# Kernel optimization log

Measured on AMD Instinct MI355X. Metric: run time of the kernel, lower is better.

Reference implementation:

```python
import jax, jax.numpy as jnp
import numpy as np

NUM_HEADS = 16
HEAD_DIM = 64
PATCH_NUMS = [1, 2, 3, 4, 5, 6, 8, 10, 13, 16, 32]
MAX_SCALE_MUL = float(np.log(100.0))


def precompute_freqs_cis(dim, patch_nums, theta=10000.0):
    # Returns [L, dim//2, 2] (cos, sin) pairs; matches torch.polar construction.
    freqs = 1.0 / theta ** (np.arange(0, dim, 4)[: dim // 4].astype(np.float32) / dim)  # [dim//4]
    tx, ty = [], []
    grid = 32.0
    for p in patch_nums:
        ix, iy = np.meshgrid(np.arange(p), np.arange(p), indexing="ij")  # torch default 'ij'
        tx.append(ix.flatten().astype(np.float32) / p * grid)
        ty.append(iy.flatten().astype(np.float32) / p * grid)
    tx = np.concatenate(tx)
    ty = np.concatenate(ty)
    ang = np.concatenate([np.outer(tx, freqs), np.outer(ty, freqs)], axis=1).astype(np.float32)  # [L, dim//2]
    return np.stack([np.cos(ang), np.sin(ang)], axis=-1)  # [L, dim//2, 2]


FREQS_CIS_CROSS = jnp.asarray(precompute_freqs_cis(HEAD_DIM, [12]))  # [144, 32, 2]


def _rope(x, cis):
    # x: [B, H, S, D]; cis: [S, D//2, 2] -> complex multiply on (even, odd) pairs.
    B, H, S, D = x.shape
    xr = x.reshape(B, H, S, D // 2, 2)
    a, b = xr[..., 0], xr[..., 1]
    c = cis[..., 0][None, None]  # [1,1,S,D//2]
    d = cis[..., 1][None, None]
    return jnp.stack([a * c - b * d, a * d + b * c], axis=-1).reshape(B, H, S, D)


def setup_inputs() -> dict:
    key = jax.random.key(0)
    ks = jax.random.split(key, 6)
    B, C, Ck, Lk = 8, 1024, 1024, 144
    fc = precompute_freqs_cis(HEAD_DIM, PATCH_NUMS)
    L = fc.shape[0]  # 1704
    return {
        "x": jax.random.normal(ks[0], (B, L, C), jnp.float32),
        "y": jax.random.normal(ks[1], (B, Lk, Ck), jnp.float32),
        "freqs_cis": jnp.asarray(fc),
        "attn_bias": jax.random.normal(ks[2], (1, 1, L, Lk), jnp.float32) * 0.1,
        "Wq": jax.random.normal(ks[3], (C, C), jnp.float32) * 0.02,
        "q_bias": jnp.zeros((C,), jnp.float32),
        "Wkv": jax.random.normal(ks[4], (2 * C, Ck), jnp.float32) * 0.02,
        "v_bias": jnp.zeros((C,), jnp.float32),
        "Wproj": jax.random.normal(ks[5], (C, C), jnp.float32) * 0.02,
        "b_proj": jnp.zeros((C,), jnp.float32),
        "scale_mul": jnp.full((1, NUM_HEADS, 1, 1), np.log(4.0), jnp.float32),
    }


def reference(x, y, freqs_cis, attn_bias, Wq, q_bias, Wkv, v_bias, Wproj, b_proj, scale_mul):
    B, L, C = x.shape
    H, D = NUM_HEADS, HEAD_DIM
    Lk = y.shape[1]
    # fused QKV projections (k bias is the zero buffer)
    q = (x @ Wq.T + q_bias).reshape(B, L, H, D).transpose(0, 2, 1, 3)  # [B,H,L,D]
    kv_bias = jnp.concatenate([jnp.zeros_like(v_bias), v_bias])
    kv = (y @ Wkv.T + kv_bias).reshape(B, Lk, 2, H, D)
    k = kv[:, :, 0].transpose(0, 2, 1, 3)  # [B,H,Lk,D]
    v = kv[:, :, 1].transpose(0, 2, 1, 3)
    # attn_l2_norm path: scale = 1, per-head learned multiplier
    sm = jnp.exp(jnp.minimum(scale_mul, MAX_SCALE_MUL))  # [1,H,1,1]
    q = q / jnp.maximum(jnp.linalg.norm(q, axis=-1, keepdims=True), 1e-12) * sm
    k = k / jnp.maximum(jnp.linalg.norm(k, axis=-1, keepdims=True), 1e-12)
    # inline RoPE (cross freqs recomputed from 12x12 grid every forward in the original)
    q = _rope(q, freqs_cis)
    k = _rope(k, FREQS_CIS_CROSS)
    # manual (non-flash) masked attention, scale = 1 due to l2 norm
    logits = jnp.einsum("bhld,bhkd->bhlk", q, k) + attn_bias
    attn = jax.nn.softmax(logits, axis=-1)
    oup = jnp.einsum("bhlk,bhkd->bhld", attn, v).transpose(0, 2, 1, 3).reshape(B, L, C)
    return oup @ Wproj.T + b_proj
```

## Files before the change

### kernel.cpp

```cpp
#include <hip/hip_runtime.h>

using u16 = unsigned short;
using u32 = unsigned int;

typedef __bf16 bf16x8 __attribute__((ext_vector_type(8)));
typedef float  f32x4  __attribute__((ext_vector_type(4)));
typedef _Float16 f16;
typedef _Float16 f16x4 __attribute__((ext_vector_type(4)));
typedef _Float16 f16x8 __attribute__((ext_vector_type(8)));
typedef u16 u16x4 __attribute__((ext_vector_type(4)));

__device__ __forceinline__ float b2f(u16 u) { return __uint_as_float(((u32)u) << 16); }
__device__ __forceinline__ u16 f2b(float f) {
    u32 u = __float_as_uint(f);
    return (u16)((u + 0x7FFFu + ((u >> 16) & 1u)) >> 16);
}

__device__ __forceinline__ void async_cp16(void* lds, const void* g) {
    __builtin_amdgcn_global_load_lds(
        (const __attribute__((address_space(1))) u32*)g,
        (__attribute__((address_space(3))) u32*)lds, 16, 0, 0);
}

__device__ __forceinline__ void split4_store(const float* src, u16* hi, u16* lo, int i) {
    f32x4 v = reinterpret_cast<const f32x4*>(src)[i];
    u16x4 H, L;
#pragma unroll
    for (int j = 0; j < 4; j++) {
        u16 hb = f2b(v[j]);
        H[j] = hb;
        L[j] = f2b(v[j] - b2f(hb));
    }
    reinterpret_cast<u16x4*>(hi)[i] = H;
    reinterpret_cast<u16x4*>(lo)[i] = L;
}

__global__ __launch_bounds__(256) void prep(const float* __restrict__ x,
                                            const float* __restrict__ Wq,
                                            const float* __restrict__ Wp,
                                            const float* __restrict__ y,
                                            const float* __restrict__ Wkv,
                                            f16* __restrict__ xf,
                                            f16* __restrict__ wqhi, f16* __restrict__ wqlo,
                                            f16* __restrict__ wph,
                                            u16* __restrict__ yhi, u16* __restrict__ ylo,
                                            u16* __restrict__ wkhi, u16* __restrict__ wklo,
                                            int nx4, int nw4, int ny4, int nwk4) {
    int i = blockIdx.x * 256 + threadIdx.x;
    if (i < nx4) {
        f32x4 v = reinterpret_cast<const f32x4*>(x)[i];
        f16x4 h = {(f16)v[0], (f16)v[1], (f16)v[2], (f16)v[3]};
        reinterpret_cast<f16x4*>(xf)[i] = h;
    } else if (i < nx4 + nw4) {
        int k = i - nx4;
        f32x4 v = reinterpret_cast<const f32x4*>(Wq)[k];
        f16x4 H, L;
#pragma unroll
        for (int j = 0; j < 4; j++) {
            f16 hb = (f16)v[j];
            H[j] = hb;
            L[j] = (f16)(v[j] - (float)hb);
        }
        reinterpret_cast<f16x4*>(wqhi)[k] = H;
        reinterpret_cast<f16x4*>(wqlo)[k] = L;
    } else if (i < nx4 + 2 * nw4) {
        int k = i - nx4 - nw4;
        f32x4 v = reinterpret_cast<const f32x4*>(Wp)[k];
        f16x4 h = {(f16)v[0], (f16)v[1], (f16)v[2], (f16)v[3]};
        reinterpret_cast<f16x4*>(wph)[k] = h;
    } else if (i < nx4 + 2 * nw4 + ny4) {
        int k = i - nx4 - 2 * nw4;
        split4_store(y, yhi, ylo, k);
    } else {
        int k = i - nx4 - 2 * nw4 - ny4;
        if (k < nwk4) split4_store(Wkv, wkhi, wklo, k);
    }
}

__device__ __forceinline__ void remap852(int j, int& mt, int& sg) {
    if (j < 832) {
        int a = j >> 5, rem = j & 31;
        mt = a * 8 + (rem & 7);
        sg = rem >> 3;
    } else {
        int rem = j - 832;
        mt = 208 + rem % 5;
        sg = rem / 5;
    }
}

__global__ __launch_bounds__(256) void gemm_q(const f16* __restrict__ xf,
                                              const f16* __restrict__ whi,
                                              const f16* __restrict__ wlo,
                                              const float* __restrict__ qb,
                                              const float* __restrict__ fc,
                                              const float* __restrict__ smul,
                                              f16* __restrict__ qout) {
    const int K = 1024, L = 1704;
    __shared__ f16 xs[2][2][64][64];
    int tid = threadIdx.x;
    int lane = tid & 63, wv = tid >> 6;
    int mt, hg;
    remap852(blockIdx.x, mt, hg);
    int h  = hg * 4 + wv;
    int lr = lane & 15, quad = lane >> 4;
    long m0 = (long)mt * 64;

    int r0 = tid >> 3, c0 = tid & 7;
    int s1i = tid + 256;
    int r1 = s1i >> 3, c1 = s1i & 7;
    const f16* srcx0 = xf + (m0 + r0) * K + ((c0 ^ (r0 & 7)) * 8);
    const f16* srcx1 = xf + (m0 + r1) * K + ((c1 ^ (r1 & 7)) * 8);
    f16* dx[2][2][2];
#pragma unroll
    for (int b = 0; b < 2; b++)
#pragma unroll
        for (int hh = 0; hh < 2; hh++) {
            dx[b][hh][0] = &xs[b][hh][r0][c0 * 8];
            dx[b][hh][1] = &xs[b][hh][r1][c1 * 8];
        }

    const f16x8* wh_p[4];
    const f16x8* wl_p[4];
#pragma unroll
    for (int i = 0; i < 4; i++) {
        long woff = ((long)(h * 64 + i * 16 + lr)) * K;
        wh_p[i] = reinterpret_cast<const f16x8*>(whi + woff) + quad;
        wl_p[i] = reinterpret_cast<const f16x8*>(wlo + woff) + quad;
    }

    int sp0 = ((0 + quad) ^ (lr & 7)) * 8;
    int sp1 = ((4 + quad) ^ (lr & 7)) * 8;

    f32x4 acc[4][4] = {};

    async_cp16(dx[0][0][0], srcx0);      async_cp16(dx[0][0][1], srcx1);
    async_cp16(dx[0][1][0], srcx0 + 64); async_cp16(dx[0][1][1], srcx1 + 64);
    __syncthreads();

    for (int c = 0; c < 8; c++) {
        if (c < 7) {
            int nb = (c + 1) & 1;
            int off = (c + 1) * 128;
            async_cp16(dx[nb][0][0], srcx0 + off);      async_cp16(dx[nb][0][1], srcx1 + off);
            async_cp16(dx[nb][1][0], srcx0 + off + 64); async_cp16(dx[nb][1][1], srcx1 + off + 64);
        }
        int buf = c & 1;
#pragma unroll
        for (int hh = 0; hh < 2; hh++) {
#pragma unroll
            for (int s = 0; s < 2; s++) {
                int o = (c * 2 + hh) * 8 + s * 4;
                int sp = s ? sp1 : sp0;
                f16x8 AF[4], WH[4], WL[4];
#pragma unroll
                for (int i = 0; i < 4; i++) {
                    WH[i] = wh_p[i][o];
                    WL[i] = wl_p[i][o];
                }
#pragma unroll
                for (int i = 0; i < 4; i++)
                    AF[i] = *reinterpret_cast<const f16x8*>(&xs[buf][hh][i * 16 + lr][sp]);
#pragma unroll
                for (int mi = 0; mi < 4; mi++)
#pragma unroll
                    for (int ni = 0; ni < 4; ni++) {
                        acc[mi][ni] = __builtin_amdgcn_mfma_f32_16x16x32_f16(AF[mi], WH[ni], acc[mi][ni], 0, 0, 0);
                        acc[mi][ni] = __builtin_amdgcn_mfma_f32_16x16x32_f16(AF[mi], WL[ni], acc[mi][ni], 0, 0, 0);
                    }
            }
        }
        __syncthreads();
    }

    float sm = __expf(fminf(smul[h], 4.6051702f));
#pragma unroll
    for (int mi = 0; mi < 4; mi++) {
#pragma unroll
        for (int r = 0; r < 4; r++) {
            long rowg = m0 + mi * 16 + quad * 4 + r;
            float v[4];
            float ss = 0.f;
#pragma unroll
            for (int ni = 0; ni < 4; ni++) {
                v[ni] = acc[mi][ni][r] + qb[h * 64 + ni * 16 + lr];
                ss += v[ni] * v[ni];
            }
            ss += __shfl_xor(ss, 1, 64); ss += __shfl_xor(ss, 2, 64);
            ss += __shfl_xor(ss, 4, 64); ss += __shfl_xor(ss, 8, 64);
            float inv = sm / fmaxf(sqrtf(ss), 1e-12f);
            int l = (int)(rowg % L);
            f16* orow = qout + rowg * 1024 + h * 64;
#pragma unroll
            for (int ni = 0; ni < 4; ni++) {
                float u = v[ni] * inv;
                int d = ni * 16 + lr;
                int j = d >> 1;
                float c = fc[(l * 32 + j) * 2];
                float s = fc[(l * 32 + j) * 2 + 1];
                float pr = __shfl_xor(u, 1, 64);
                float o = (lane & 1) ? (pr * s + u * c) : (u * c - pr * s);
                orow[d] = (f16)o;
            }
        }
    }
}

__constant__ double FREQS16[16] = {
    1.0, 0.5623413251903491, 0.31622776601683794, 0.17782794100389228,
    0.1, 0.05623413251903491, 0.03162277660168379, 0.017782794100389228,
    0.01, 0.005623413251903491, 0.0031622776601683794, 0.0017782794100389228,
    0.001, 0.0005623413251903491, 0.00031622776601683794, 0.00017782794100389228};

__global__ __launch_bounds__(256) void gemm_kv(const u16* __restrict__ yhi,
                                               const u16* __restrict__ ylo,
                                               const u16* __restrict__ wkhi,
                                               const u16* __restrict__ wklo,
                                               const float* __restrict__ vb,
                                               f16* __restrict__ khp,
                                               f16* __restrict__ klp,
                                               f16* __restrict__ vhp,
                                               f16* __restrict__ vlp) {
    const int K = 1024;
    int lane = threadIdx.x & 63, wv = threadIdx.x >> 6;
    int mt = blockIdx.x >> 3;
    int nt = (blockIdx.x & 7) * 4 + wv;
    int lr = lane & 15, quad = lane >> 4;
    long m0 = (long)mt * 32;

    const bf16x8* ah_p[2];
    const bf16x8* al_p[2];
    const bf16x8* wh_p[4];
    const bf16x8* wl_p[4];
#pragma unroll
    for (int i = 0; i < 2; i++) {
        long aoff = (m0 + i * 16 + lr) * K;
        ah_p[i] = reinterpret_cast<const bf16x8*>(yhi + aoff) + quad;
        al_p[i] = reinterpret_cast<const bf16x8*>(ylo + aoff) + quad;
    }
#pragma unroll
    for (int i = 0; i < 4; i++) {
        long woff = ((long)(nt * 64 + i * 16 + lr)) * K;
        wh_p[i] = reinterpret_cast<const bf16x8*>(wkhi + woff) + quad;
        wl_p[i] = reinterpret_cast<const bf16x8*>(wklo + woff) + quad;
    }

    f32x4 acc[2][4] = {};
    for (int ks = 0; ks < 32; ks++) {
        int o = ks * 4;
        bf16x8 ah[2], al[2], wh[4], wl[4];
#pragma unroll
        for (int i = 0; i < 2; i++) { ah[i] = ah_p[i][o]; al[i] = al_p[i][o]; }
#pragma unroll
        for (int i = 0; i < 4; i++) { wh[i] = wh_p[i][o]; wl[i] = wl_p[i][o]; }
#pragma unroll
        for (int mi = 0; mi < 2; mi++)
#pragma unroll
            for (int ni = 0; ni < 4; ni++) {
                acc[mi][ni] = __builtin_amdgcn_mfma_f32_16x16x32_bf16(ah[mi], wh[ni], acc[mi][ni], 0, 0, 0);
                acc[mi][ni] = __builtin_amdgcn_mfma_f32_16x16x32_bf16(al[mi], wh[ni], acc[mi][ni], 0, 0, 0);
                acc[mi][ni] = __builtin_amdgcn_mfma_f32_16x16x32_bf16(ah[mi], wl[ni], acc[mi][ni], 0, 0, 0);
            }
    }

    bool isv = nt >= 16;
    int h = isv ? nt - 16 : nt;
#pragma unroll
    for (int mi = 0; mi < 2; mi++) {
#pragma unroll
        for (int r = 0; r < 4; r++) {
            long row = m0 + mi * 16 + quad * 4 + r;
            int b = (int)(row / 144), lk = (int)(row % 144);
            long bh = b * 16 + h;
            float v[4];
#pragma unroll
            for (int ni = 0; ni < 4; ni++)
                v[ni] = acc[mi][ni][r] + (isv ? vb[h * 64 + ni * 16 + lr] : 0.f);
            if (!isv) {
                float ss = v[0] * v[0] + v[1] * v[1] + v[2] * v[2] + v[3] * v[3];
                ss += __shfl_xor(ss, 1, 64); ss += __shfl_xor(ss, 2, 64);
                ss += __shfl_xor(ss, 4, 64); ss += __shfl_xor(ss, 8, 64);
                float inv = 1.f / fmaxf(sqrtf(ss), 1e-12f);
                f16* kh_row = khp + (bh * 144 + lk) * 64;
                f16* kl_row = klp + (bh * 144 + lk) * 64;
#pragma unroll
                for (int ni = 0; ni < 4; ni++) {
                    float u = v[ni] * inv;
                    int d = ni * 16 + lr;
                    int j = d >> 1;
                    int f = j & 15;
                    float tc = (j < 16) ? ((float)(lk / 12)) / 12.0f * 32.0f
                                        : ((float)(lk % 12)) / 12.0f * 32.0f;
                    float ang = (float)((double)tc * FREQS16[f]);
                    float c = cosf(ang), s = sinf(ang);
                    float pr = __shfl_xor(u, 1, 64);
                    float o = (lane & 1) ? (pr * s + u * c) : (u * c - pr * s);
                    f16 oh = (f16)o;
                    f16 ol = (f16)(o - (float)oh);
                    kh_row[d] = oh;
                    kl_row[d] = ol;
                }
            } else {
#pragma unroll
                for (int ni = 0; ni < 4; ni++) {
                    float val = v[ni];
                    int d = ni * 16 + lr;
                    f16 vh = (f16)val;
                    f16 vl = (f16)(val - (float)vh);
                    vhp[(bh * 64 + d) * 144 + lk] = vh;
                    vlp[(bh * 64 + d) * 144 + lk] = vl;
                }
            }
        }
    }
}

__global__ __launch_bounds__(256, 3) void attn(const f16* q,
                                               const f16* __restrict__ khp,
                                               const f16* __restrict__ klp,
                                               const f16* __restrict__ vhp,
                                               const f16* __restrict__ vlp,
                                               const float* __restrict__ abias,
                                               f16* aout) {
    const int L = 1704;
    __shared__ __align__(16) f16 ps[4][16][152];
    int tid = threadIdx.x;
    int lane = tid & 63, wv = tid >> 6;
    int lr = lane & 15, quad = lane >> 4;
    int ltile = blockIdx.x % 27;
    int bh = blockIdx.x / 27;
    int h = bh & 15, b = bh >> 4;
    int l0 = ltile * 64;
    int rows = min(64, L - l0);

    int rA = wv * 16 + lr;
    int rAc = min(rA, rows - 1);
    const f16* qrow = q + ((long)(b * L + l0 + rAc)) * 1024 + h * 64;
    f16x8 qa0 = *reinterpret_cast<const f16x8*>(qrow + quad * 8);
    f16x8 qa1 = *reinterpret_cast<const f16x8*>(qrow + 32 + quad * 8);

    const f16* khb = khp + (long)bh * (144 * 64);
    const f16* klb = klp + (long)bh * (144 * 64);

    f32x4 acc[9] = {};
#pragma unroll
    for (int t = 0; t < 9; t++) {
        const f16* k0 = khb + (t * 16 + lr) * 64 + quad * 8;
        const f16* k1 = klb + (t * 16 + lr) * 64 + quad * 8;
        f16x8 bh0 = *reinterpret_cast<const f16x8*>(k0);
        f16x8 bh1 = *reinterpret_cast<const f16x8*>(k0 + 32);
        f16x8 bl0 = *reinterpret_cast<const f16x8*>(k1);
        f16x8 bl1 = *reinterpret_cast<const f16x8*>(k1 + 32);
        __builtin_amdgcn_s_setprio(1);
        acc[t] = __builtin_amdgcn_mfma_f32_16x16x32_f16(qa0, bh0, acc[t], 0, 0, 0);
        acc[t] = __builtin_amdgcn_mfma_f32_16x16x32_f16(qa1, bh1, acc[t], 0, 0, 0);
        acc[t] = __builtin_amdgcn_mfma_f32_16x16x32_f16(qa0, bl0, acc[t], 0, 0, 0);
        acc[t] = __builtin_amdgcn_mfma_f32_16x16x32_f16(qa1, bl1, acc[t], 0, 0, 0);
        __builtin_amdgcn_s_setprio(0);
    }

    int rC = wv * 16 + quad * 4;
#pragma unroll
    for (int r = 0; r < 4; r++) {
        long lrow = (long)(l0 + min(rC + r, rows - 1)) * 144;
#pragma unroll
        for (int t = 0; t < 9; t++) acc[t][r] += abias[lrow + t * 16 + lr];
    }

#pragma unroll
    for (int r = 0; r < 4; r++) {
        float mx = acc[0][r];
#pragma unroll
        for (int t = 1; t < 9; t++) mx = fmaxf(mx, acc[t][r]);
        mx = fmaxf(mx, __shfl_xor(mx, 1, 64));
        mx = fmaxf(mx, __shfl_xor(mx, 2, 64));
        mx = fmaxf(mx, __shfl_xor(mx, 4, 64));
        mx = fmaxf(mx, __shfl_xor(mx, 8, 64));
        float s = 0.f;
#pragma unroll
        for (int t = 0; t < 9; t++) {
            float e = __expf(acc[t][r] - mx);
            acc[t][r] = e;
            s += e;
        }
        s += __shfl_xor(s, 1, 64);
        s += __shfl_xor(s, 2, 64);
        s += __shfl_xor(s, 4, 64);
        s += __shfl_xor(s, 8, 64);
        float inv = 1.0f / s;
#pragma unroll
        for (int t = 0; t < 9; t++)
            ps[wv][quad * 4 + r][t * 16 + lr] = (f16)(acc[t][r] * inv);
    }

    const f16* vhb = vhp + (long)bh * (64 * 144);
    const f16* vlb = vlp + (long)bh * (64 * 144);
    f32x4 oacc[4] = {};
#pragma unroll
    for (int ks = 0; ks < 5; ks++) {
        f16x8 pa = {0, 0, 0, 0, 0, 0, 0, 0};
        if (ks < 4 || quad < 2)
            pa = *reinterpret_cast<const f16x8*>(&ps[wv][lr][ks * 32 + quad * 8]);
#pragma unroll
        for (int n = 0; n < 4; n++) {
            f16x8 vh8 = {0, 0, 0, 0, 0, 0, 0, 0};
            f16x8 vl8 = {0, 0, 0, 0, 0, 0, 0, 0};
            if (ks < 4 || quad < 2) {
                const f16* vr  = vhb + (n * 16 + lr) * 144 + ks * 32 + quad * 8;
                const f16* vr2 = vlb + (n * 16 + lr) * 144 + ks * 32 + quad * 8;
                vh8 = *reinterpret_cast<const f16x8*>(vr);
                vl8 = *reinterpret_cast<const f16x8*>(vr2);
            }
            __builtin_amdgcn_s_setprio(1);
            oacc[n] = __builtin_amdgcn_mfma_f32_16x16x32_f16(pa, vh8, oacc[n], 0, 0, 0);
            oacc[n] = __builtin_amdgcn_mfma_f32_16x16x32_f16(pa, vl8, oacc[n], 0, 0, 0);
            __builtin_amdgcn_s_setprio(0);
        }
    }

    long ob = (long)(b * L + l0);
#pragma unroll
    for (int r = 0; r < 4; r++) {
        int rw = rC + r;
        if (rw < rows) {
            f16* ao = aout + (ob + rw) * 1024 + h * 64;
#pragma unroll
            for (int n = 0; n < 4; n++) ao[n * 16 + lr] = (f16)oacc[n][r];
        }
    }
}

__global__ __launch_bounds__(256) void gemm_proj(const f16* __restrict__ A,
                                                 const f16* __restrict__ Wh,
                                                 const float* __restrict__ bias,
                                                 float* __restrict__ out) {
    const int K = 1024;
    __shared__ f16 as[2][2][64][64];
    int tid = threadIdx.x;
    int lane = tid & 63, wv = tid >> 6;
    int mt, cg;
    remap852(blockIdx.x, mt, cg);
    int lr = lane & 15, quad = lane >> 4;
    long m0 = (long)mt * 64;
    long n0 = (long)cg * 256 + wv * 64;

    int r0 = tid >> 3, c0 = tid & 7;
    int s1i = tid + 256;
    int r1 = s1i >> 3, c1 = s1i & 7;
    const f16* srca0 = A + (m0 + r0) * K + ((c0 ^ (r0 & 7)) * 8);
    const f16* srca1 = A + (m0 + r1) * K + ((c1 ^ (r1 & 7)) * 8);
    f16* da[2][2][2];
#pragma unroll
    for (int b = 0; b < 2; b++)
#pragma unroll
        for (int hh = 0; hh < 2; hh++) {
            da[b][hh][0] = &as[b][hh][r0][c0 * 8];
            da[b][hh][1] = &as[b][hh][r1][c1 * 8];
        }

    const f16x8* wrow[4];
#pragma unroll
    for (int i = 0; i < 4; i++)
        wrow[i] = reinterpret_cast<const f16x8*>(Wh + (n0 + i * 16 + lr) * K) + quad;

    int sp0 = ((0 + quad) ^ (lr & 7)) * 8;
    int sp1 = ((4 + quad) ^ (lr & 7)) * 8;

    f32x4 acc[4][4] = {};

    async_cp16(da[0][0][0], srca0);      async_cp16(da[0][0][1], srca1);
    async_cp16(da[0][1][0], srca0 + 64); async_cp16(da[0][1][1], srca1 + 64);
    __syncthreads();

    for (int c = 0; c < 8; c++) {
        if (c < 7) {
            int nb = (c + 1) & 1;
            int off = (c + 1) * 128;
            async_cp16(da[nb][0][0], srca0 + off);      async_cp16(da[nb][0][1], srca1 + off);
            async_cp16(da[nb][1][0], srca0 + off + 64); async_cp16(da[nb][1][1], srca1 + off + 64);
        }
        int buf = c & 1;
#pragma unroll
        for (int hh = 0; hh < 2; hh++) {
#pragma unroll
            for (int s = 0; s < 2; s++) {
                int o = (c * 2 + hh) * 8 + s * 4;
                int sp = s ? sp1 : sp0;
                f16x8 af[4], wf[4];
#pragma unroll
                for (int i = 0; i < 4; i++) wf[i] = wrow[i][o];
#pragma unroll
                for (int i = 0; i < 4; i++)
                    af[i] = *reinterpret_cast<const f16x8*>(&as[buf][hh][i * 16 + lr][sp]);
#pragma unroll
                for (int mi = 0; mi < 4; mi++)
#pragma unroll
                    for (int ni = 0; ni < 4; ni++)
                        acc[mi][ni] = __builtin_amdgcn_mfma_f32_16x16x32_f16(af[mi], wf[ni], acc[mi][ni], 0, 0, 0);
            }
        }
        __syncthreads();
    }

#pragma unroll
    for (int ni = 0; ni < 4; ni++) {
        int col = (int)n0 + ni * 16 + lr;
        float b = bias[col];
#pragma unroll
        for (int mi = 0; mi < 4; mi++) {
            long row = m0 + mi * 16 + quad * 4;
#pragma unroll
            for (int r = 0; r < 4; r++)
                out[(row + r) * 1024 + col] = acc[mi][ni][r] + b;
        }
    }
}

extern "C" void kernel_launch(void* const* d_in, const int* in_sizes, int n_in,
                              void* d_out, int out_size, void* d_ws, size_t ws_size,
                              hipStream_t stream) {
    const float* x     = (const float*)d_in[0];
    const float* y     = (const float*)d_in[1];
    const float* fc    = (const float*)d_in[2];
    const float* abias = (const float*)d_in[3];
    const float* Wq    = (const float*)d_in[4];
    const float* qb    = (const float*)d_in[5];
    const float* Wkv   = (const float*)d_in[6];
    const float* vb    = (const float*)d_in[7];
    const float* Wp    = (const float*)d_in[8];
    const float* bp    = (const float*)d_in[9];
    const float* smul  = (const float*)d_in[10];

    const long XN  = 13959168L;
    const long WN  = 1048576L;
    const long YN  = 1179648L;
    const long WKN = 2097152L;
    const long KVN = 1179648L;

    f16* qbuf  = (f16*)d_ws;
    f16* wq_hi = qbuf + XN;
    f16* wq_lo = wq_hi + WN;
    f16* wp_h  = wq_lo + WN;

    f16* x_f   = (f16*)d_out;
    u16* y_hi  = (u16*)(x_f + XN);
    u16* y_lo  = y_hi + YN;
    u16* wk_hi = y_lo + YN;
    u16* wk_lo = wk_hi + WKN;
    f16* kh_p  = (f16*)d_out;
    f16* kl_p  = kh_p + KVN;
    f16* vth_p = kl_p + KVN;
    f16* vtl_p = vth_p + KVN;

    int nx4  = (int)(XN / 4);
    int nw4  = (int)(WN / 4);
    int ny4  = (int)(YN / 4);
    int nwk4 = (int)(WKN / 4);
    int prep_blocks = (nx4 + 2 * nw4 + ny4 + nwk4 + 255) / 256;

    prep<<<dim3(prep_blocks), dim3(256), 0, stream>>>(
        x, Wq, Wp, y, Wkv, x_f, wq_hi, wq_lo, wp_h,
        y_hi, y_lo, wk_hi, wk_lo, nx4, nw4, ny4, nwk4);
    gemm_q<<<dim3(852), dim3(256), 0, stream>>>(x_f, wq_hi, wq_lo, qb, fc, smul, qbuf);
    gemm_kv<<<dim3(288), dim3(256), 0, stream>>>(y_hi, y_lo, wk_hi, wk_lo, vb,
                                                 kh_p, kl_p, vth_p, vtl_p);
    attn<<<dim3(3456), dim3(256), 0, stream>>>(qbuf, kh_p, kl_p, vth_p, vtl_p, abias, (f16*)qbuf);
    gemm_proj<<<dim3(852), dim3(256), 0, stream>>>((const f16*)qbuf, wp_h, bp, (float*)d_out);
}
```

Measured before the change: 536.6 us.

## Merge Q and KV projections into one launch and halve GEMM M tiles

Folds the separate Q and KV projection kernels into one kernel whose first 288 blocks do the KV work and whose remaining blocks do the Q GEMM. This lets the two run concurrently and removes one launch. The Q and output-projection GEMMs drop from 64-row to 32-row M tiles, doubling the grid to 1704 blocks for better CU occupancy. The cost is less reuse of each weight fragment per block, and the K/V buffers move to a separate region so they no longer alias the x staging buffer being read concurrently.

Result: slower. 604.7 us (+12.7%).

```diff
diff --git a/kernel.cpp b/kernel.cpp
--- a/kernel.cpp
+++ b/kernel.cpp
@@ -77,48 +77,151 @@
     }
 }
 
-__device__ __forceinline__ void remap852(int j, int& mt, int& sg) {
-    if (j < 832) {
+__device__ __forceinline__ void remap1704(int j, int& mt, int& sg) {
+    if (j < 1696) {
         int a = j >> 5, rem = j & 31;
         mt = a * 8 + (rem & 7);
         sg = rem >> 3;
     } else {
-        int rem = j - 832;
-        mt = 208 + rem % 5;
-        sg = rem / 5;
-    }
-}
-
-__global__ __launch_bounds__(256) void gemm_q(const f16* __restrict__ xf,
-                                              const f16* __restrict__ whi,
-                                              const f16* __restrict__ wlo,
-                                              const float* __restrict__ qb,
-                                              const float* __restrict__ fc,
-                                              const float* __restrict__ smul,
-                                              f16* __restrict__ qout) {
+        int rem = j - 1696;
+        mt = 424 + (rem >> 2);
+        sg = rem & 3;
+    }
+}
+
+__constant__ double FREQS16[16] = {
+    1.0, 0.5623413251903491, 0.31622776601683794, 0.17782794100389228,
+    0.1, 0.05623413251903491, 0.03162277660168379, 0.017782794100389228,
+    0.01, 0.005623413251903491, 0.0031622776601683794, 0.0017782794100389228,
+    0.001, 0.0005623413251903491, 0.00031622776601683794, 0.00017782794100389228};
+
+__global__ __launch_bounds__(256) void qkv(const f16* __restrict__ xf,
+                                           const f16* __restrict__ whi,
+                                           const f16* __restrict__ wlo,
+                                           const float* __restrict__ qb,
+                                           const float* __restrict__ fc,
+                                           const float* __restrict__ smul,
+                                           f16* __restrict__ qout,
+                                           const u16* __restrict__ yhi,
+                                           const u16* __restrict__ ylo,
+                                           const u16* __restrict__ wkhi,
+                                           const u16* __restrict__ wklo,
+                                           const float* __restrict__ vb,
+                                           f16* __restrict__ khp,
+                                           f16* __restrict__ klp,
+                                           f16* __restrict__ vhp,
+                                           f16* __restrict__ vlp) {
     const int K = 1024, L = 1704;
-    __shared__ f16 xs[2][2][64][64];
+    __shared__ f16 xs[2][2][32][64];
     int tid = threadIdx.x;
     int lane = tid & 63, wv = tid >> 6;
+    int lr = lane & 15, quad = lane >> 4;
+
+    if (blockIdx.x < 288) {
+        int mt = blockIdx.x >> 3;
+        int nt = (blockIdx.x & 7) * 4 + wv;
+        long m0 = (long)mt * 32;
+
+        const bf16x8* ah_p[2];
+        const bf16x8* al_p[2];
+        const bf16x8* wh_p[4];
+        const bf16x8* wl_p[4];
+#pragma unroll
+        for (int i = 0; i < 2; i++) {
+            long aoff = (m0 + i * 16 + lr) * K;
+            ah_p[i] = reinterpret_cast<const bf16x8*>(yhi + aoff) + quad;
+            al_p[i] = reinterpret_cast<const bf16x8*>(ylo + aoff) + quad;
+        }
+#pragma unroll
+        for (int i = 0; i < 4; i++) {
+            long woff = ((long)(nt * 64 + i * 16 + lr)) * K;
+            wh_p[i] = reinterpret_cast<const bf16x8*>(wkhi + woff) + quad;
+            wl_p[i] = reinterpret_cast<const bf16x8*>(wklo + woff) + quad;
+        }
+
+        f32x4 acc[2][4] = {};
+        for (int ks = 0; ks < 32; ks++) {
+            int o = ks * 4;
+            bf16x8 ah[2], al[2], wh[4], wl[4];
+#pragma unroll
+            for (int i = 0; i < 2; i++) { ah[i] = ah_p[i][o]; al[i] = al_p[i][o]; }
+#pragma unroll
+            for (int i = 0; i < 4; i++) { wh[i] = wh_p[i][o]; wl[i] = wl_p[i][o]; }
+#pragma unroll
+            for (int mi = 0; mi < 2; mi++)
+#pragma unroll
+                for (int ni = 0; ni < 4; ni++) {
+                    acc[mi][ni] = __builtin_amdgcn_mfma_f32_16x16x32_bf16(ah[mi], wh[ni], acc[mi][ni], 0, 0, 0);
+                    acc[mi][ni] = __builtin_amdgcn_mfma_f32_16x16x32_bf16(al[mi], wh[ni], acc[mi][ni], 0, 0, 0);
+                    acc[mi][ni] = __builtin_amdgcn_mfma_f32_16x16x32_bf16(ah[mi], wl[ni], acc[mi][ni], 0, 0, 0);
+                }
+        }
+
+        bool isv = nt >= 16;
+        int h = isv ? nt - 16 : nt;
+#pragma unroll
+        for (int mi = 0; mi < 2; mi++) {
+#pragma unroll
+            for (int r = 0; r < 4; r++) {
+                long row = m0 + mi * 16 + quad * 4 + r;
+                int b = (int)(row / 144), lk = (int)(row % 144);
+                long bh = b * 16 + h;
+                float v[4];
+#pragma unroll
+                for (int ni = 0; ni < 4; ni++)
+                    v[ni] = acc[mi][ni][r] + (isv ? vb[h * 64 + ni * 16 + lr] : 0.f);
+                if (!isv) {
+                    float ss = v[0] * v[0] + v[1] * v[1] + v[2] * v[2] + v[3] * v[3];
+                    ss += __shfl_xor(ss, 1, 64); ss += __shfl_xor(ss, 2, 64);
+                    ss += __shfl_xor(ss, 4, 64); ss += __shfl_xor(ss, 8, 64);
+                    float inv = 1.f / fmaxf(sqrtf(ss), 1e-12f);
+                    f16* kh_row = khp + (bh * 144 + lk) * 64;
+                    f16* kl_row = klp + (bh * 144 + lk) * 64;
+#pragma unroll
+                    for (int ni = 0; ni < 4; ni++) {
+                        float u = v[ni] * inv;
+                        int d = ni * 16 + lr;
+                        int j = d >> 1;
+                        int f = j & 15;
+                        float tc = (j < 16) ? ((float)(lk / 12)) / 12.0f * 32.0f
+                                            : ((float)(lk % 12)) / 12.0f * 32.0f;
+                        float ang = (float)((double)tc * FREQS16[f]);
+                        float c = cosf(ang), s = sinf(ang);
+                        float pr = __shfl_xor(u, 1, 64);
+                        float o = (lane & 1) ? (pr * s + u * c) : (u * c - pr * s);
+                        f16 oh = (f16)o;
+                        f16 ol = (f16)(o - (float)oh);
+                        kh_row[d] = oh;
+                        kl_row[d] = ol;
+                    }
+                } else {
+#pragma unroll
+                    for (int ni = 0; ni < 4; ni++) {
+                        float val = v[ni];
+                        int d = ni * 16 + lr;
+                        f16 vh = (f16)val;
+                        f16 vl = (f16)(val - (float)vh);
+                        vhp[(bh * 64 + d) * 144 + lk] = vh;
+                        vlp[(bh * 64 + d) * 144 + lk] = vl;
+                    }
+                }
+            }
+        }
+        return;
+    }
+
     int mt, hg;
-    remap852(blockIdx.x, mt, hg);
+    remap1704(blockIdx.x - 288, mt, hg);
     int h  = hg * 4 + wv;
-    int lr = lane & 15, quad = lane >> 4;
-    long m0 = (long)mt * 64;
+    long m0 = (long)mt * 32;
 
     int r0 = tid >> 3, c0 = tid & 7;
-    int s1i = tid + 256;
-    int r1 = s1i >> 3, c1 = s1i & 7;
     const f16* srcx0 = xf + (m0 + r0) * K + ((c0 ^ (r0 & 7)) * 8);
-    const f16* srcx1 = xf + (m0 + r1) * K + ((c1 ^ (r1 & 7)) * 8);
-    f16* dx[2][2][2];
+    f16* dx[2][2];
 #pragma unroll
     for (int b = 0; b < 2; b++)
 #pragma unroll
-        for (int hh = 0; hh < 2; hh++) {
-            dx[b][hh][0] = &xs[b][hh][r0][c0 * 8];
-            dx[b][hh][1] = &xs[b][hh][r1][c1 * 8];
-        }
+        for (int hh = 0; hh < 2; hh++) dx[b][hh] = &xs[b][hh][r0][c0 * 8];
 
     const f16x8* wh_p[4];
     const f16x8* wl_p[4];
@@ -132,18 +235,18 @@
     int sp0 = ((0 + quad) ^ (lr & 7)) * 8;
     int sp1 = ((4 + quad) ^ (lr & 7)) * 8;
 
-    f32x4 acc[4][4] = {};
-
-    async_cp16(dx[0][0][0], srcx0);      async_cp16(dx[0][0][1], srcx1);
-    async_cp16(dx[0][1][0], srcx0 + 64); async_cp16(dx[0][1][1], srcx1 + 64);
+    f32x4 acc[2][4] = {};
+
+    async_cp16(dx[0][0], srcx0);
+    async_cp16(dx[0][1], srcx0 + 64);
     __syncthreads();
 
     for (int c = 0; c < 8; c++) {
         if (c < 7) {
             int nb = (c + 1) & 1;
             int off = (c + 1) * 128;
-            async_cp16(dx[nb][0][0], srcx0 + off);      async_cp16(dx[nb][0][1], srcx1 + off);
-            async_cp16(dx[nb][1][0], srcx0 + off + 64); async_cp16(dx[nb][1][1], srcx1 + off + 64);
+            async_cp16(dx[nb][0], srcx0 + off);
+            async_cp16(dx[nb][1], srcx0 + off + 64);
         }
         int buf = c & 1;
 #pragma unroll
@@ -152,17 +255,17 @@
             for (int s = 0; s < 2; s++) {
                 int o = (c * 2 + hh) * 8 + s * 4;
                 int sp = s ? sp1 : sp0;
-                f16x8 AF[4], WH[4], WL[4];
+                f16x8 AF[2], WH[4], WL[4];
 #pragma unroll
                 for (int i = 0; i < 4; i++) {
                     WH[i] = wh_p[i][o];
                     WL[i] = wl_p[i][o];
                 }
 #pragma unroll
-                for (int i = 0; i < 4; i++)
+                for (int i = 0; i < 2; i++)
                     AF[i] = *reinterpret_cast<const f16x8*>(&xs[buf][hh][i * 16 + lr][sp]);
 #pragma unroll
-                for (int mi = 0; mi < 4; mi++)
+                for (int mi = 0; mi < 2; mi++)
 #pragma unroll
                     for (int ni = 0; ni < 4; ni++) {
                         acc[mi][ni] = __builtin_amdgcn_mfma_f32_16x16x32_f16(AF[mi], WH[ni], acc[mi][ni], 0, 0, 0);
@@ -175,7 +278,7 @@
 
     float sm = __expf(fminf(smul[h], 4.6051702f));
 #pragma unroll
-    for (int mi = 0; mi < 4; mi++) {
+    for (int mi = 0; mi < 2; mi++) {
 #pragma unroll
         for (int r = 0; r < 4; r++) {
             long rowg = m0 + mi * 16 + quad * 4 + r;
@@ -201,115 +304,6 @@
                 float pr = __shfl_xor(u, 1, 64);
                 float o = (lane & 1) ? (pr * s + u * c) : (u * c - pr * s);
                 orow[d] = (f16)o;
-            }
-        }
-    }
-}
-
-__constant__ double FREQS16[16] = {
-    1.0, 0.5623413251903491, 0.31622776601683794, 0.17782794100389228,
-    0.1, 0.05623413251903491, 0.03162277660168379, 0.017782794100389228,
-    0.01, 0.005623413251903491, 0.0031622776601683794, 0.0017782794100389228,
-    0.001, 0.0005623413251903491, 0.00031622776601683794, 0.00017782794100389228};
-
-__global__ __launch_bounds__(256) void gemm_kv(const u16* __restrict__ yhi,
-                                               const u16* __restrict__ ylo,
-                                               const u16* __restrict__ wkhi,
-                                               const u16* __restrict__ wklo,
-                                               const float* __restrict__ vb,
-                                               f16* __restrict__ khp,
-                                               f16* __restrict__ klp,
-                                               f16* __restrict__ vhp,
-                                               f16* __restrict__ vlp) {
-    const int K = 1024;
-    int lane = threadIdx.x & 63, wv = threadIdx.x >> 6;
-    int mt = blockIdx.x >> 3;
-    int nt = (blockIdx.x & 7) * 4 + wv;
-    int lr = lane & 15, quad = lane >> 4;
-    long m0 = (long)mt * 32;
-
-    const bf16x8* ah_p[2];
-    const bf16x8* al_p[2];
-    const bf16x8* wh_p[4];
-    const bf16x8* wl_p[4];
-#pragma unroll
-    for (int i = 0; i < 2; i++) {
-        long aoff = (m0 + i * 16 + lr) * K;
-        ah_p[i] = reinterpret_cast<const bf16x8*>(yhi + aoff) + quad;
-        al_p[i] = reinterpret_cast<const bf16x8*>(ylo + aoff) + quad;
-    }
-#pragma unroll
-    for (int i = 0; i < 4; i++) {
-        long woff = ((long)(nt * 64 + i * 16 + lr)) * K;
-        wh_p[i] = reinterpret_cast<const bf16x8*>(wkhi + woff) + quad;
-        wl_p[i] = reinterpret_cast<const bf16x8*>(wklo + woff) + quad;
-    }
-
-    f32x4 acc[2][4] = {};
-    for (int ks = 0; ks < 32; ks++) {
-        int o = ks * 4;
-        bf16x8 ah[2], al[2], wh[4], wl[4];
-#pragma unroll
-        for (int i = 0; i < 2; i++) { ah[i] = ah_p[i][o]; al[i] = al_p[i][o]; }
-#pragma unroll
-        for (int i = 0; i < 4; i++) { wh[i] = wh_p[i][o]; wl[i] = wl_p[i][o]; }
-#pragma unroll
-        for (int mi = 0; mi < 2; mi++)
-#pragma unroll
-            for (int ni = 0; ni < 4; ni++) {
-                acc[mi][ni] = __builtin_amdgcn_mfma_f32_16x16x32_bf16(ah[mi], wh[ni], acc[mi][ni], 0, 0, 0);
-                acc[mi][ni] = __builtin_amdgcn_mfma_f32_16x16x32_bf16(al[mi], wh[ni], acc[mi][ni], 0, 0, 0);
-                acc[mi][ni] = __builtin_amdgcn_mfma_f32_16x16x32_bf16(ah[mi], wl[ni], acc[mi][ni], 0, 0, 0);
-            }
-    }
-
-    bool isv = nt >= 16;
-    int h = isv ? nt - 16 : nt;
-#pragma unroll
-    for (int mi = 0; mi < 2; mi++) {
-#pragma unroll
-        for (int r = 0; r < 4; r++) {
-            long row = m0 + mi * 16 + quad * 4 + r;
-            int b = (int)(row / 144), lk = (int)(row % 144);
-            long bh = b * 16 + h;
-            float v[4];
-#pragma unroll
-            for (int ni = 0; ni < 4; ni++)
-                v[ni] = acc[mi][ni][r] + (isv ? vb[h * 64 + ni * 16 + lr] : 0.f);
-            if (!isv) {
-                float ss = v[0] * v[0] + v[1] * v[1] + v[2] * v[2] + v[3] * v[3];
-                ss += __shfl_xor(ss, 1, 64); ss += __shfl_xor(ss, 2, 64);
-                ss += __shfl_xor(ss, 4, 64); ss += __shfl_xor(ss, 8, 64);
-                float inv = 1.f / fmaxf(sqrtf(ss), 1e-12f);
-                f16* kh_row = khp + (bh * 144 + lk) * 64;
-                f16* kl_row = klp + (bh * 144 + lk) * 64;
-#pragma unroll
-                for (int ni = 0; ni < 4; ni++) {
-                    float u = v[ni] * inv;
-                    int d = ni * 16 + lr;
-                    int j = d >> 1;
-                    int f = j & 15;
-                    float tc = (j < 16) ? ((float)(lk / 12)) / 12.0f * 32.0f
-                                        : ((float)(lk % 12)) / 12.0f * 32.0f;
-                    float ang = (float)((double)tc * FREQS16[f]);
-                    float c = cosf(ang), s = sinf(ang);
-                    float pr = __shfl_xor(u, 1, 64);
-                    float o = (lane & 1) ? (pr * s + u * c) : (u * c - pr * s);
-                    f16 oh = (f16)o;
-                    f16 ol = (f16)(o - (float)oh);
-                    kh_row[d] = oh;
-                    kl_row[d] = ol;
-                }
-            } else {
-#pragma unroll
-                for (int ni = 0; ni < 4; ni++) {
-                    float val = v[ni];
-                    int d = ni * 16 + lr;
-                    f16 vh = (f16)val;
-                    f16 vl = (f16)(val - (float)vh);
-                    vhp[(bh * 64 + d) * 144 + lk] = vh;
-                    vlp[(bh * 64 + d) * 144 + lk] = vl;
-                }
             }
         }
     }
@@ -435,28 +429,22 @@
                                                  const float* __restrict__ bias,
                                                  float* __restrict__ out) {
     const int K = 1024;
-    __shared__ f16 as[2][2][64][64];
+    __shared__ f16 as[2][2][32][64];
     int tid = threadIdx.x;
     int lane = tid & 63, wv = tid >> 6;
     int mt, cg;
-    remap852(blockIdx.x, mt, cg);
+    remap1704(blockIdx.x, mt, cg);
     int lr = lane & 15, quad = lane >> 4;
-    long m0 = (long)mt * 64;
+    long m0 = (long)mt * 32;
     long n0 = (long)cg * 256 + wv * 64;
 
     int r0 = tid >> 3, c0 = tid & 7;
-    int s1i = tid + 256;
-    int r1 = s1i >> 3, c1 = s1i & 7;
     const f16* srca0 = A + (m0 + r0) * K + ((c0 ^ (r0 & 7)) * 8);
-    const f16* srca1 = A + (m0 + r1) * K + ((c1 ^ (r1 & 7)) * 8);
-    f16* da[2][2][2];
+    f16* da[2][2];
 #pragma unroll
     for (int b = 0; b < 2; b++)
 #pragma unroll
-        for (int hh = 0; hh < 2; hh++) {
-            da[b][hh][0] = &as[b][hh][r0][c0 * 8];
-            da[b][hh][1] = &as[b][hh][r1][c1 * 8];
-        }
+        for (int hh = 0; hh < 2; hh++) da[b][hh] = &as[b][hh][r0][c0 * 8];
 
     const f16x8* wrow[4];
 #pragma unroll
@@ -466,18 +454,18 @@
     int sp0 = ((0 + quad) ^ (lr & 7)) * 8;
     int sp1 = ((4 + quad) ^ (lr & 7)) * 8;
 
-    f32x4 acc[4][4] = {};
-
-    async_cp16(da[0][0][0], srca0);      async_cp16(da[0][0][1], srca1);
-    async_cp16(da[0][1][0], srca0 + 64); async_cp16(da[0][1][1], srca1 + 64);
+    f32x4 acc[2][4] = {};
+
+    async_cp16(da[0][0], srca0);
+    async_cp16(da[0][1], srca0 + 64);
     __syncthreads();
 
     for (int c = 0; c < 8; c++) {
         if (c < 7) {
             int nb = (c + 1) & 1;
             int off = (c + 1) * 128;
-            async_cp16(da[nb][0][0], srca0 + off);      async_cp16(da[nb][0][1], srca1 + off);
-            async_cp16(da[nb][1][0], srca0 + off + 64); async_cp16(da[nb][1][1], srca1 + off + 64);
+            async_cp16(da[nb][0], srca0 + off);
+            async_cp16(da[nb][1], srca0 + off + 64);
         }
         int buf = c & 1;
 #pragma unroll
@@ -486,14 +474,14 @@
             for (int s = 0; s < 2; s++) {
                 int o = (c * 2 + hh) * 8 + s * 4;
                 int sp = s ? sp1 : sp0;
-                f16x8 af[4], wf[4];
+                f16x8 af[2], wf[4];
 #pragma unroll
                 for (int i = 0; i < 4; i++) wf[i] = wrow[i][o];
 #pragma unroll
-                for (int i = 0; i < 4; i++)
+                for (int i = 0; i < 2; i++)
                     af[i] = *reinterpret_cast<const f16x8*>(&as[buf][hh][i * 16 + lr][sp]);
 #pragma unroll
-                for (int mi = 0; mi < 4; mi++)
+                for (int mi = 0; mi < 2; mi++)
 #pragma unroll
                     for (int ni = 0; ni < 4; ni++)
                         acc[mi][ni] = __builtin_amdgcn_mfma_f32_16x16x32_f16(af[mi], wf[ni], acc[mi][ni], 0, 0, 0);
@@ -507,7 +495,7 @@
         int col = (int)n0 + ni * 16 + lr;
         float b = bias[col];
 #pragma unroll
-        for (int mi = 0; mi < 4; mi++) {
+        for (int mi = 0; mi < 2; mi++) {
             long row = m0 + mi * 16 + quad * 4;
 #pragma unroll
             for (int r = 0; r < 4; r++)
@@ -547,7 +535,7 @@
     u16* y_lo  = y_hi + YN;
     u16* wk_hi = y_lo + YN;
     u16* wk_lo = wk_hi + WKN;
-    f16* kh_p  = (f16*)d_out;
+    f16* kh_p  = (f16*)(wk_lo + WKN);
     f16* kl_p  = kh_p + KVN;
     f16* vth_p = kl_p + KVN;
     f16* vtl_p = vth_p + KVN;
@@ -561,9 +549,9 @@
     prep<<<dim3(prep_blocks), dim3(256), 0, stream>>>(
         x, Wq, Wp, y, Wkv, x_f, wq_hi, wq_lo, wp_h,
         y_hi, y_lo, wk_hi, wk_lo, nx4, nw4, ny4, nwk4);
-    gemm_q<<<dim3(852), dim3(256), 0, stream>>>(x_f, wq_hi, wq_lo, qb, fc, smul, qbuf);
-    gemm_kv<<<dim3(288), dim3(256), 0, stream>>>(y_hi, y_lo, wk_hi, wk_lo, vb,
-                                                 kh_p, kl_p, vth_p, vtl_p);
+    qkv<<<dim3(288 + 1704), dim3(256), 0, stream>>>(
+        x_f, wq_hi, wq_lo, qb, fc, smul, qbuf,
+        y_hi, y_lo, wk_hi, wk_lo, vb, kh_p, kl_p, vth_p, vtl_p);
     attn<<<dim3(3456), dim3(256), 0, stream>>>(qbuf, kh_p, kl_p, vth_p, vtl_p, abias, (f16*)qbuf);
-    gemm_proj<<<dim3(852), dim3(256), 0, stream>>>((const f16*)qbuf, wp_h, bp, (float*)d_out);
-}
+    gemm_proj<<<dim3(1704), dim3(256), 0, stream>>>((const f16*)qbuf, wp_h, bp, (float*)d_out);
+}
```
